# Performance work log

Hardware: AMD Instinct MI355X
Metric: run time of the kernel (lower is better)

The kernel has to match this reference:

```python
import jax, jax.numpy as jnp
import numpy as np

N_NODES = 50000
N_EDGES = 800000
NFEAT = 128
NHID = 128
NCLASS = 64


def _gcn_conv(x, W, b, src, dst, ew, n_nodes):
    # PyG GCNConv: h = x @ W; out[i] = sum_{(j->i)} norm_ji * h[j] + b
    # norm = deg^-1/2[src] * w * deg^-1/2[dst], deg from scatter of w on dst
    h = x @ W  # [N, out]
    deg = jax.ops.segment_sum(ew, dst, num_segments=n_nodes)
    dinv = jnp.where(deg > 0, deg ** -0.5, 0.0)
    norm = dinv[src] * ew * dinv[dst]  # [E]
    msg = h[src] * norm[:, None]  # [E, out] gather + scale
    out = jax.ops.segment_sum(msg, dst, num_segments=n_nodes)
    return out + b


def setup_inputs() -> dict:
    key = jax.random.key(0)
    ks = jax.random.split(key, 10)
    x = jax.random.normal(ks[0], (N_NODES, NFEAT), dtype=jnp.float32)
    edge_index = jax.random.randint(ks[1], (2, N_EDGES), 0, N_NODES, dtype=jnp.int64)
    edge_weight = jax.random.uniform(ks[2], (N_EDGES,), dtype=jnp.float32)
    def glorot(k, shape):
        lim = float(np.sqrt(6.0 / (shape[0] + shape[1])))
        return jax.random.uniform(k, shape, dtype=jnp.float32, minval=-lim, maxval=lim)
    return {
        "x": x,
        "edge_index": edge_index,
        "edge_weight": edge_weight,
        "W1": glorot(ks[3], (NFEAT, NHID)),
        "b1": jnp.zeros((NHID,), jnp.float32),
        "W2": glorot(ks[4], (NHID, NHID)),
        "b2": jnp.zeros((NHID,), jnp.float32),
        "fcW": glorot(ks[5], (NHID, NCLASS)),
        "fcb": jnp.zeros((NCLASS,), jnp.float32),
    }


def reference(x, edge_index, edge_weight, W1, b1, W2, b2, fcW, fcb):
    n = x.shape[0]
    # add self-loops (PyG GCNConv default, self-loop weight = 1)
    loop = jnp.arange(n, dtype=edge_index.dtype)
    src = jnp.concatenate([edge_index[0], loop])
    dst = jnp.concatenate([edge_index[1], loop])
    ew = jnp.concatenate([edge_weight, jnp.ones((n,), edge_weight.dtype)])
    # eval mode: dropout is identity; use_ln / layer_norm_first are False
    h = jax.nn.relu(_gcn_conv(x, W1, b1, src, dst, ew, n))
    h = jax.nn.relu(_gcn_conv(h, W2, b2, src, dst, ew, n))
    logits = h @ fcW + fcb
    return jax.nn.log_softmax(logits, axis=1)
```

## Files before the change

kernel.cpp:

```cpp
#include <hip/hip_runtime.h>
#include <hip/hip_bf16.h>


typedef __attribute__((ext_vector_type(8))) short short8;
typedef __attribute__((ext_vector_type(4))) float floatx4;

static __device__ __forceinline__ float bfu(unsigned short u) {
    return __uint_as_float(((unsigned)u) << 16);
}
static __device__ __forceinline__ unsigned short f2bu(float f) {
    unsigned u = __float_as_uint(f);
    unsigned r = (u + 0x7FFFu + ((u >> 16) & 1u)) >> 16;
    return (unsigned short)r;
}


__global__ void k_detect(const int* __restrict__ ei, int* flag) {
    __shared__ int nz;
    if (threadIdx.x == 0) nz = 0;
    __syncthreads();
    if (ei[2 * threadIdx.x + 1] != 0) atomicOr(&nz, 1);
    __syncthreads();
    if (threadIdx.x == 0) flag[0] = (nz == 0) ? 1 : 0;
}


__global__ void k_init(unsigned* packed, int N) {
    int i = blockIdx.x * 256 + threadIdx.x;
    if (i < N) packed[i] = 0u;
}


__global__ void k_edge(const int* __restrict__ ei, const int* __restrict__ flag,
                       const float* __restrict__ ew,
                       unsigned* __restrict__ packed, int2* __restrict__ ell, int E) {
    int e = blockIdx.x * 256 + threadIdx.x;
    if (e >= E) return;
    int s_, d;
    if (flag[0]) {
        const long long* p = (const long long*)ei;
        s_ = (int)p[e];
        d  = (int)p[(long)E + e];
    } else {
        s_ = ei[e];
        d  = ei[E + e];
    }
    float w = ew[e];
    unsigned enc = (unsigned)(w * 524288.0f + 0.5f);
    unsigned old = atomicAdd(packed + d, (1u << 25) | enc);
    unsigned rank = old >> 25;
    if (rank < 64) ell[(long)d * 64 + rank] = make_int2(s_, __float_as_int(w));
}


__global__ void k_dinv(const unsigned* __restrict__ packed, float* dinv, int N) {
    int i = blockIdx.x * 256 + threadIdx.x;
    if (i < N) {
        float deg = 1.0f + (float)(packed[i] & 0x1FFFFFFu) * (1.0f / 524288.0f);
        dinv[i] = rsqrtf(deg);
    }
}


__global__ void k_pack(const float* __restrict__ W, unsigned short* __restrict__ wp) {
    int idx = blockIdx.x * 256 + threadIdx.x;
    if (idx >= 16384) return;
    int j = idx & 7, l = (idx >> 3) & 63, n = (idx >> 9) & 7, kt = idx >> 12;
    int k = kt * 32 + ((l >> 4) << 3) + j;
    int c = n * 16 + (l & 15);
    wp[idx] = f2bu(W[k * 128 + c]);
}


__global__ void k_pack_fc(const float* __restrict__ W, unsigned short* __restrict__ wp) {
    int idx = blockIdx.x * 256 + threadIdx.x;
    if (idx >= 8192) return;
    int j = idx & 7, l = (idx >> 3) & 63, n = (idx >> 9) & 3, kt = idx >> 11;
    int k = kt * 32 + ((l >> 4) << 3) + j;
    int c = n * 16 + (l & 15);
    float w = W[k * 64 + c];
    unsigned short h = f2bu(w);
    wp[idx] = h;
    wp[8192 + idx] = f2bu(w - bfu(h));
}


__global__ __launch_bounds__(256)
void k_gemm_mfma(const float* __restrict__ A, const unsigned short* __restrict__ wp,
                 unsigned short* __restrict__ C, int M) {
    __shared__ unsigned short wPack[16384];
    int t = threadIdx.x;
    {
        const float4* g = (const float4*)wp;
        float4* s = (float4*)wPack;
#pragma unroll
        for (int j = 0; j < 8; j++) s[t + j * 256] = g[t + j * 256];
    }
    __syncthreads();
    int w = t >> 6, lane = t & 63;
    int quad = lane >> 4, m = lane & 15;
    int nchunks = (M + 63) >> 6;
    for (int chunk = blockIdx.x; chunk < nchunks; chunk += gridDim.x) {
        int rowbase = chunk * 64 + w * 16;
        floatx4 acc[8];
#pragma unroll
        for (int n = 0; n < 8; n++) acc[n] = (floatx4){0.f, 0.f, 0.f, 0.f};
        int arow = rowbase + m;
        if (arow > M - 1) arow = M - 1;
        const float* ap = A + (long)arow * 128 + quad * 8;
#pragma unroll
        for (int kt = 0; kt < 4; kt++) {
            float4 f0 = *(const float4*)(ap + kt * 32);
            float4 f1 = *(const float4*)(ap + kt * 32 + 4);
            float av[8] = {f0.x, f0.y, f0.z, f0.w, f1.x, f1.y, f1.z, f1.w};
            short8 hi, lo;
#pragma unroll
            for (int j = 0; j < 8; j++) {
                unsigned short h = f2bu(av[j]);
                hi[j] = (short)h;
                lo[j] = (short)f2bu(av[j] - bfu(h));
            }
#pragma unroll
            for (int n = 0; n < 8; n++) {
                short8 b = *(const short8*)&wPack[(((kt * 8 + n) * 64) + lane) * 8];
                acc[n] = __builtin_amdgcn_mfma_f32_16x16x32_bf16(hi, b, acc[n], 0, 0, 0);
                acc[n] = __builtin_amdgcn_mfma_f32_16x16x32_bf16(lo, b, acc[n], 0, 0, 0);
            }
        }
#pragma unroll
        for (int r = 0; r < 4; r++) {
            int row = rowbase + quad * 4 + r;
            if (row < M) {
#pragma unroll
                for (int n = 0; n < 8; n++) {
                    C[(long)row * 128 + n * 16 + m] = f2bu(acc[n][r]);
                }
            }
        }
    }
}


__global__ __launch_bounds__(64)
void k_agg(const unsigned short* __restrict__ h, const int2* __restrict__ ell,
           const unsigned* __restrict__ packed, const float* __restrict__ dinv,
           const float* __restrict__ bias, float* __restrict__ out, int N) {
    __shared__ int2 sL[64];
    int i = blockIdx.x;
    int l = threadIdx.x;
    const unsigned* h32 = (const unsigned*)h;
    float dn = dinv[i];
    unsigned sv = h32[(long)i * 64 + l];
    float2 bv = ((const float2*)bias)[l];
    int cnt = min(64u, packed[i] >> 25);
    if (l < cnt) {
        int2 pp = ell[(long)i * 64 + l];
        sL[l] = make_int2(pp.x, __float_as_int(dinv[pp.x] * __int_as_float(pp.y)));
    }
    __syncthreads();
    float sx = 0.f, sy = 0.f;
    int j = 0;
    for (; j + 8 <= cnt; j += 8) {
        unsigned v[8]; float nr[8];
#pragma unroll
        for (int u = 0; u < 8; u++) {
            int2 pp = sL[j + u];
            v[u] = h32[(long)pp.x * 64 + l];
            nr[u] = __int_as_float(pp.y);
        }
#pragma unroll
        for (int u = 0; u < 8; u++) {
            sx += nr[u] * bfu((unsigned short)(v[u] & 0xffff));
            sy += nr[u] * bfu((unsigned short)(v[u] >> 16));
        }
    }
    for (; j < cnt; j++) {
        int2 pp = sL[j];
        unsigned v0 = h32[(long)pp.x * 64 + l];
        float nr0 = __int_as_float(pp.y);
        sx += nr0 * bfu((unsigned short)(v0 & 0xffff));
        sy += nr0 * bfu((unsigned short)(v0 >> 16));
    }
    float dn2 = dn * dn;
    float accx = bv.x + dn2 * bfu((unsigned short)(sv & 0xffff)) + dn * sx;
    float accy = bv.y + dn2 * bfu((unsigned short)(sv >> 16)) + dn * sy;
    ((float2*)out)[(long)i * 64 + l] =
        make_float2(fmaxf(accx, 0.f), fmaxf(accy, 0.f));
}


__global__ __launch_bounds__(256)
void k_fc_lsm(const float* __restrict__ h, const unsigned short* __restrict__ wp,
              const float* __restrict__ fcb, float* __restrict__ out, int N) {
    __shared__ unsigned short wS[16384];
    int t = threadIdx.x;
    {
        const float4* g = (const float4*)wp;
        float4* s = (float4*)wS;
#pragma unroll
        for (int j = 0; j < 8; j++) s[t + j * 256] = g[t + j * 256];
    }
    __syncthreads();
    int w = t >> 6, lane = t & 63;
    int quad = lane >> 4, m = lane & 15;
    int nchunks = (N + 63) >> 6;
    for (int chunk = blockIdx.x; chunk < nchunks; chunk += gridDim.x) {
        int rowbase = chunk * 64 + w * 16;
        floatx4 acc[4];
#pragma unroll
        for (int n = 0; n < 4; n++) acc[n] = (floatx4){0.f, 0.f, 0.f, 0.f};
        int arow = rowbase + m;
        if (arow > N - 1) arow = N - 1;
        const float* ap = h + (long)arow * 128 + quad * 8;
#pragma unroll
        for (int kt = 0; kt < 4; kt++) {
            float4 f0 = *(const float4*)(ap + kt * 32);
            float4 f1 = *(const float4*)(ap + kt * 32 + 4);
            float av[8] = {f0.x, f0.y, f0.z, f0.w, f1.x, f1.y, f1.z, f1.w};
            short8 hi, lo;
#pragma unroll
            for (int j = 0; j < 8; j++) {
                unsigned short hb = f2bu(av[j]);
                hi[j] = (short)hb;
                lo[j] = (short)f2bu(av[j] - bfu(hb));
            }
#pragma unroll
            for (int n = 0; n < 4; n++) {
                int fo = (((kt * 4 + n) * 64) + lane) * 8;
                short8 bh = *(const short8*)&wS[fo];
                short8 bl = *(const short8*)&wS[8192 + fo];
                acc[n] = __builtin_amdgcn_mfma_f32_16x16x32_bf16(hi, bh, acc[n], 0, 0, 0);
                acc[n] = __builtin_amdgcn_mfma_f32_16x16x32_bf16(lo, bh, acc[n], 0, 0, 0);
                acc[n] = __builtin_amdgcn_mfma_f32_16x16x32_bf16(hi, bl, acc[n], 0, 0, 0);
            }
        }
#pragma unroll
        for (int r = 0; r < 4; r++) {
            int row = rowbase + quad * 4 + r;
            float v0 = acc[0][r] + fcb[m];
            float v1 = acc[1][r] + fcb[16 + m];
            float v2 = acc[2][r] + fcb[32 + m];
            float v3 = acc[3][r] + fcb[48 + m];
            float mx = fmaxf(fmaxf(v0, v1), fmaxf(v2, v3));
#pragma unroll
            for (int msk = 1; msk < 16; msk <<= 1) mx = fmaxf(mx, __shfl_xor(mx, msk, 64));
            float s_ = __expf(v0 - mx) + __expf(v1 - mx) + __expf(v2 - mx) + __expf(v3 - mx);
#pragma unroll
            for (int msk = 1; msk < 16; msk <<= 1) s_ += __shfl_xor(s_, msk, 64);
            float ls = mx + __logf(s_);
            if (row < N) {
                float* op = out + (long)row * 64 + m;
                op[0]  = v0 - ls;
                op[16] = v1 - ls;
                op[32] = v2 - ls;
                op[48] = v3 - ls;
            }
        }
    }
}


extern "C" void kernel_launch(void* const* d_in, const int* in_sizes, int n_in,
                              void* d_out, int out_size, void* d_ws, size_t ws_size,
                              hipStream_t stream) {
    const float* x   = (const float*)d_in[0];
    const int*   ei  = (const int*)d_in[1];
    const float* ew  = (const float*)d_in[2];
    const float* W1  = (const float*)d_in[3];
    const float* b1  = (const float*)d_in[4];
    const float* W2  = (const float*)d_in[5];
    const float* b2  = (const float*)d_in[6];
    const float* fcW = (const float*)d_in[7];
    const float* fcb = (const float*)d_in[8];
    float* out = (float*)d_out;

    int N = in_sizes[0] / 128;
    int E = in_sizes[2];

    char* p = (char*)d_ws;
    auto alloc = [&](size_t b) -> void* {
        void* r = (void*)p;
        p += (b + 255) & ~(size_t)255;
        return r;
    };
    int*      flag   = (int*)alloc(4);
    unsigned* packed = (unsigned*)alloc((size_t)N * 4);
    float*    dinv   = (float*)alloc((size_t)N * 4);
    int2*     ell    = (int2*)alloc((size_t)N * 64 * 8);
    unsigned short* wp1 = (unsigned short*)alloc(16384 * 2);
    unsigned short* wp2 = (unsigned short*)alloc(16384 * 2);
    unsigned short* wpf = (unsigned short*)alloc(16384 * 2);
    unsigned short* hbuf = (unsigned short*)alloc((size_t)N * 128 * 2);
    float* aggbuf = (float*)alloc((size_t)N * 128 * 4);

    int gN = (N + 255) / 256, gE = (E + 255) / 256;
    k_detect<<<1, 1024, 0, stream>>>(ei, flag);
    k_init<<<gN, 256, 0, stream>>>(packed, N);
    k_edge<<<gE, 256, 0, stream>>>(ei, flag, ew, packed, ell, E);
    k_dinv<<<gN, 256, 0, stream>>>(packed, dinv, N);
    k_pack<<<64, 256, 0, stream>>>(W1, wp1);
    k_pack<<<64, 256, 0, stream>>>(W2, wp2);
    k_pack_fc<<<32, 256, 0, stream>>>(fcW, wpf);

    int nchunks = (N + 63) / 64;
    k_gemm_mfma<<<nchunks, 256, 0, stream>>>(x, wp1, hbuf, N);
    k_agg<<<N, 64, 0, stream>>>(hbuf, ell, packed, dinv, b1, aggbuf, N);
    k_gemm_mfma<<<nchunks, 256, 0, stream>>>(aggbuf, wp2, hbuf, N);
    k_agg<<<N, 64, 0, stream>>>(hbuf, ell, packed, dinv, b2, aggbuf, N);
    k_fc_lsm<<<nchunks, 256, 0, stream>>>(aggbuf, wpf, fcb, out, N);
}
```

Before: 241.9 us.

## Merge setup kernels and interleave edge build with first GEMM in one launch

Combines the zero-init, int64-detect and three weight-packing kernels into a single setup launch. A second kernel interleaves the first-layer GEMM blocks with the edge-scatter blocks in one grid so the compute-bound MFMA work and the atomic-heavy ELL construction can share the GPU at once. This cuts the launch count and idle tails between small kernels. The cost is that edge blocks still allocate the 32KB LDS array, which may limit occupancy for the scatter part.

```diff
diff --git a/kernel.cpp b/kernel.cpp
--- a/kernel.cpp
+++ b/kernel.cpp
@@ -15,66 +15,14 @@
 }
 
 
-__global__ void k_detect(const int* __restrict__ ei, int* flag) {
-    __shared__ int nz;
-    if (threadIdx.x == 0) nz = 0;
-    __syncthreads();
-    if (ei[2 * threadIdx.x + 1] != 0) atomicOr(&nz, 1);
-    __syncthreads();
-    if (threadIdx.x == 0) flag[0] = (nz == 0) ? 1 : 0;
-}
-
-
-__global__ void k_init(unsigned* packed, int N) {
-    int i = blockIdx.x * 256 + threadIdx.x;
-    if (i < N) packed[i] = 0u;
-}
-
-
-__global__ void k_edge(const int* __restrict__ ei, const int* __restrict__ flag,
-                       const float* __restrict__ ew,
-                       unsigned* __restrict__ packed, int2* __restrict__ ell, int E) {
-    int e = blockIdx.x * 256 + threadIdx.x;
-    if (e >= E) return;
-    int s_, d;
-    if (flag[0]) {
-        const long long* p = (const long long*)ei;
-        s_ = (int)p[e];
-        d  = (int)p[(long)E + e];
-    } else {
-        s_ = ei[e];
-        d  = ei[E + e];
-    }
-    float w = ew[e];
-    unsigned enc = (unsigned)(w * 524288.0f + 0.5f);
-    unsigned old = atomicAdd(packed + d, (1u << 25) | enc);
-    unsigned rank = old >> 25;
-    if (rank < 64) ell[(long)d * 64 + rank] = make_int2(s_, __float_as_int(w));
-}
-
-
-__global__ void k_dinv(const unsigned* __restrict__ packed, float* dinv, int N) {
-    int i = blockIdx.x * 256 + threadIdx.x;
-    if (i < N) {
-        float deg = 1.0f + (float)(packed[i] & 0x1FFFFFFu) * (1.0f / 524288.0f);
-        dinv[i] = rsqrtf(deg);
-    }
-}
-
-
-__global__ void k_pack(const float* __restrict__ W, unsigned short* __restrict__ wp) {
-    int idx = blockIdx.x * 256 + threadIdx.x;
-    if (idx >= 16384) return;
+static __device__ __forceinline__ void d_pack128(const float* W, unsigned short* wp, int idx) {
     int j = idx & 7, l = (idx >> 3) & 63, n = (idx >> 9) & 7, kt = idx >> 12;
     int k = kt * 32 + ((l >> 4) << 3) + j;
     int c = n * 16 + (l & 15);
     wp[idx] = f2bu(W[k * 128 + c]);
 }
 
-
-__global__ void k_pack_fc(const float* __restrict__ W, unsigned short* __restrict__ wp) {
-    int idx = blockIdx.x * 256 + threadIdx.x;
-    if (idx >= 8192) return;
+static __device__ __forceinline__ void d_pack_fc(const float* W, unsigned short* wp, int idx) {
     int j = idx & 7, l = (idx >> 3) & 63, n = (idx >> 9) & 3, kt = idx >> 11;
     int k = kt * 32 + ((l >> 4) << 3) + j;
     int c = n * 16 + (l & 15);
@@ -82,6 +30,124 @@
     unsigned short h = f2bu(w);
     wp[idx] = h;
     wp[8192 + idx] = f2bu(w - bfu(h));
+}
+
+
+__global__ __launch_bounds__(256)
+void k_setup(const int* __restrict__ ei, int* flag, unsigned* packed, int N, int gN,
+             const float* __restrict__ W1, unsigned short* wp1,
+             const float* __restrict__ W2, unsigned short* wp2,
+             const float* __restrict__ fcW, unsigned short* wpf) {
+    int b = blockIdx.x, t = threadIdx.x;
+    if (b < gN) {
+        int i = b * 256 + t;
+        if (i < N) packed[i] = 0u;
+    } else if (b == gN) {
+        __shared__ int nz;
+        if (t == 0) nz = 0;
+        __syncthreads();
+        int acc = 0;
+#pragma unroll
+        for (int r = 0; r < 4; r++) acc |= ei[2 * (t + 256 * r) + 1];
+        if (acc != 0) atomicOr(&nz, 1);
+        __syncthreads();
+        if (t == 0) flag[0] = (nz == 0) ? 1 : 0;
+    } else if (b < gN + 65) {
+        d_pack128(W1, wp1, (b - gN - 1) * 256 + t);
+    } else if (b < gN + 129) {
+        d_pack128(W2, wp2, (b - gN - 65) * 256 + t);
+    } else {
+        d_pack_fc(fcW, wpf, (b - gN - 129) * 256 + t);
+    }
+}
+
+
+__global__ void k_dinv(const unsigned* __restrict__ packed, float* dinv, int N) {
+    int i = blockIdx.x * 256 + threadIdx.x;
+    if (i < N) {
+        float deg = 1.0f + (float)(packed[i] & 0x1FFFFFFu) * (1.0f / 524288.0f);
+        dinv[i] = rsqrtf(deg);
+    }
+}
+
+
+__global__ __launch_bounds__(256)
+void k_edge_gemm(const int* __restrict__ ei, const int* __restrict__ flag,
+                 const float* __restrict__ ew,
+                 unsigned* __restrict__ packed, int2* __restrict__ ell, int E,
+                 const float* __restrict__ A, const unsigned short* __restrict__ wp,
+                 unsigned short* __restrict__ C, int M, int nchunks, int kfac) {
+    __shared__ unsigned short wPack[16384];
+    int b = blockIdx.x, t = threadIdx.x;
+    int q = b / kfac, rem = b - q * kfac;
+    bool isGemm = (rem == 0) && (q < nchunks);
+
+    if (!isGemm) {
+        int eb = b - min(q + (rem > 0 ? 1 : 0), nchunks);
+        int e = eb * 256 + t;
+        if (e >= E) return;
+        int s_, d;
+        if (flag[0]) {
+            const long long* p = (const long long*)ei;
+            s_ = (int)p[e];
+            d  = (int)p[(long)E + e];
+        } else {
+            s_ = ei[e];
+            d  = ei[E + e];
+        }
+        float w = ew[e];
+        unsigned enc = (unsigned)(w * 524288.0f + 0.5f);
+        unsigned old = atomicAdd(packed + d, (1u << 25) | enc);
+        unsigned rank = old >> 25;
+        if (rank < 64) ell[(long)d * 64 + rank] = make_int2(s_, __float_as_int(w));
+        return;
+    }
+
+    {
+        const float4* g = (const float4*)wp;
+        float4* s = (float4*)wPack;
+#pragma unroll
+        for (int j = 0; j < 8; j++) s[t + j * 256] = g[t + j * 256];
+    }
+    __syncthreads();
+    int w = t >> 6, lane = t & 63;
+    int quad = lane >> 4, m = lane & 15;
+    int rowbase = q * 64 + w * 16;
+    floatx4 acc[8];
+#pragma unroll
+    for (int n = 0; n < 8; n++) acc[n] = (floatx4){0.f, 0.f, 0.f, 0.f};
+    int arow = rowbase + m;
+    if (arow > M - 1) arow = M - 1;
+    const float* ap = A + (long)arow * 128 + quad * 8;
+#pragma unroll
+    for (int kt = 0; kt < 4; kt++) {
+        float4 f0 = *(const float4*)(ap + kt * 32);
+        float4 f1 = *(const float4*)(ap + kt * 32 + 4);
+        float av[8] = {f0.x, f0.y, f0.z, f0.w, f1.x, f1.y, f1.z, f1.w};
+        short8 hi, lo;
+#pragma unroll
+        for (int j = 0; j < 8; j++) {
+            unsigned short h = f2bu(av[j]);
+            hi[j] = (short)h;
+            lo[j] = (short)f2bu(av[j] - bfu(h));
+        }
+#pragma unroll
+        for (int n = 0; n < 8; n++) {
+            short8 bfr = *(const short8*)&wPack[(((kt * 8 + n) * 64) + lane) * 8];
+            acc[n] = __builtin_amdgcn_mfma_f32_16x16x32_bf16(hi, bfr, acc[n], 0, 0, 0);
+            acc[n] = __builtin_amdgcn_mfma_f32_16x16x32_bf16(lo, bfr, acc[n], 0, 0, 0);
+        }
+    }
+#pragma unroll
+    for (int r = 0; r < 4; r++) {
+        int row = rowbase + quad * 4 + r;
+        if (row < M) {
+#pragma unroll
+            for (int n = 0; n < 8; n++) {
+                C[(long)row * 128 + n * 16 + m] = f2bu(acc[n][r]);
+            }
+        }
+    }
 }
 
 
@@ -294,16 +360,18 @@
     float* aggbuf = (float*)alloc((size_t)N * 128 * 4);
 
     int gN = (N + 255) / 256, gE = (E + 255) / 256;
-    k_detect<<<1, 1024, 0, stream>>>(ei, flag);
-    k_init<<<gN, 256, 0, stream>>>(packed, N);
-    k_edge<<<gE, 256, 0, stream>>>(ei, flag, ew, packed, ell, E);
+    int nchunks = (N + 63) / 64;
+
+    k_setup<<<gN + 161, 256, 0, stream>>>(ei, flag, packed, N, gN,
+                                          W1, wp1, W2, wp2, fcW, wpf);
+
+    int total = gE + nchunks;
+    int kfac = total / nchunks;
+    if (kfac < 2) kfac = 2;
+    k_edge_gemm<<<total, 256, 0, stream>>>(ei, flag, ew, packed, ell, E,
+                                           x, wp1, hbuf, N, nchunks, kfac);
+
     k_dinv<<<gN, 256, 0, stream>>>(packed, dinv, N);
-    k_pack<<<64, 256, 0, stream>>>(W1, wp1);
-    k_pack<<<64, 256, 0, stream>>>(W2, wp2);
-    k_pack_fc<<<32, 256, 0, stream>>>(fcW, wpf);
-
-    int nchunks = (N + 63) / 64;
-    k_gemm_mfma<<<nchunks, 256, 0, stream>>>(x, wp1, hbuf, N);
     k_agg<<<N, 64, 0, stream>>>(hbuf, ell, packed, dinv, b1, aggbuf, N);
     k_gemm_mfma<<<nchunks, 256, 0, stream>>>(aggbuf, wp2, hbuf, N);
     k_agg<<<N, 64, 0, stream>>>(hbuf, ell, packed, dinv, b2, aggbuf, N);
```

After: 245.0 us. About the same (+1.3%).
